# Kernel optimization log

Measured on AMD Instinct MI355X. Metric: run time of the kernel, lower is better.

Reference implementation:

```python
import jax, jax.numpy as jnp
import numpy as np

D_ATOM, D_MODEL, H = 128, 512, 4
D_H = D_ATOM // H
D_FF = 4 * D_ATOM
EPS = 1e-5


def _ln(x, g, b):
    m = jnp.mean(x, axis=-1, keepdims=True)
    v = jnp.mean((x - m) ** 2, axis=-1, keepdims=True)
    return (x - m) / jnp.sqrt(v + EPS) * g + b


def setup_inputs() -> dict:
    key = jax.random.key(0)
    ks = jax.random.split(key, 20)
    B, N_ATOM, N_PAIRS, N_TOK = 2, 2048, 16384, 512
    c_atom = jax.random.normal(ks[0], (B, N_ATOM, D_ATOM), dtype=jnp.float32)
    p_lm = jax.random.normal(ks[1], (B, N_PAIRS, 16), dtype=jnp.float32)
    p_lm_idx = jax.random.randint(ks[2], (B, N_PAIRS, 2), 0, N_ATOM, dtype=jnp.int32)
    token_idx = jnp.sort(jax.random.randint(ks[3], (B, N_ATOM), 0, N_TOK, dtype=jnp.int32), axis=-1)
    s = 0.05
    w = lambda k, sh: jax.random.normal(k, sh, dtype=jnp.float32) * s
    return {
        'c_atom': c_atom, 'p_lm': p_lm, 'p_lm_idx': p_lm_idx,
        'token_idx': token_idx, 'n_tokens': N_TOK,
        'ln_attn_g': jnp.ones((D_ATOM,), jnp.float32), 'ln_attn_b': jnp.zeros((D_ATOM,), jnp.float32),
        'w_q': w(ks[4], (D_ATOM, D_ATOM)), 'w_k': w(ks[5], (D_ATOM, D_ATOM)),
        'w_v': w(ks[6], (D_ATOM, D_ATOM)), 'w_g': w(ks[7], (D_ATOM, D_ATOM)),
        'w_o': w(ks[8], (D_ATOM, D_ATOM)),
        'pb_w': w(ks[9], (16, H)), 'pb_b': jnp.zeros((H,), jnp.float32),
        'ln_ff_g': jnp.ones((D_ATOM,), jnp.float32), 'ln_ff_b': jnp.zeros((D_ATOM,), jnp.float32),
        'sw_w1': w(ks[10], (D_ATOM, D_FF)), 'sw_w2': w(ks[11], (D_ATOM, D_FF)),
        'sw_w3': w(ks[12], (D_FF, D_ATOM)),
        'tok_w': w(ks[13], (D_ATOM, D_MODEL)), 'tok_b': jnp.zeros((D_MODEL,), jnp.float32),
    }


def reference(c_atom, p_lm, p_lm_idx, token_idx, n_tokens,
              ln_attn_g, ln_attn_b, w_q, w_k, w_v, w_g, w_o, pb_w, pb_b,
              ln_ff_g, ln_ff_b, sw_w1, sw_w2, sw_w3, tok_w, tok_b):
    B, N, _ = c_atom.shape
    q_n = _ln(c_atom, ln_attn_g, ln_attn_b)
    Q = (q_n @ w_q).reshape(B, N, H, D_H)
    K = (q_n @ w_k).reshape(B, N, H, D_H)
    V = (q_n @ w_v).reshape(B, N, H, D_H)
    G = q_n @ w_g  # (B, N, d_atom)

    scores = jnp.einsum('bihd,bjhd->bhij', Q, K) / jnp.sqrt(jnp.float32(D_H))

    bias = p_lm @ pb_w + pb_b  # (B, P, H)
    def scat(src, dst, b_):
        return jnp.zeros((H, N, N), b_.dtype).at[:, src, dst].set(b_.T)
    pair_bias = jax.vmap(scat)(p_lm_idx[..., 0], p_lm_idx[..., 1], bias)
    scores = scores + pair_bias

    token_mask = token_idx[:, :, None] == token_idx[:, None, :]  # (B,N,N)
    scores = jnp.where(token_mask[:, None], scores, -jnp.inf)
    attn = jax.nn.softmax(scores, axis=-1)
    attn = jnp.nan_to_num(attn)

    att_out = jnp.einsum('bhij,bjhd->bihd', attn, V).reshape(B, N, D_ATOM)
    q = c_atom + jax.nn.sigmoid(G) * (att_out @ w_o)
    h = _ln(q, ln_ff_g, ln_ff_b)
    q = q + (jax.nn.silu(h @ sw_w1) * (h @ sw_w2)) @ sw_w3
    atom_feat = q @ tok_w + tok_b  # (B, N, d_model)

    seg = (token_idx + jnp.arange(B, dtype=token_idx.dtype)[:, None] * n_tokens).reshape(-1)
    sums = jax.ops.segment_sum(atom_feat.reshape(B * N, D_MODEL), seg, num_segments=B * n_tokens)
    cnts = jax.ops.segment_sum(jnp.ones((B * N,), atom_feat.dtype), seg, num_segments=B * n_tokens)
    out = sums / jnp.maximum(cnts, 1.0)[:, None]
    return out.reshape(B, n_tokens, D_MODEL)
```

## Files before the change

### kernel.cpp

```cpp
#include <hip/hip_runtime.h>
#include <hip/hip_bf16.h>
#include <math.h>

#define B_     2
#define N_     2048
#define DA     128
#define H_     4
#define DH     32
#define DFF    512
#define DM     512
#define NT     512
#define NP     16384
#define MAXL   32
#define LDSP   136

typedef short bf16x8 __attribute__((ext_vector_type(8)));
typedef float f32x4  __attribute__((ext_vector_type(4)));

__device__ __forceinline__ short bf16r(float x) {
    union { float f; unsigned u; } v; v.f = x;
    unsigned r = v.u + 0x7FFFu + ((v.u >> 16) & 1u);
    return (short)(r >> 16);
}
__device__ __forceinline__ float bf2f(short h) {
    union { unsigned u; float f; } v;
    v.u = ((unsigned)(unsigned short)h) << 16;
    return v.f;
}

__global__ __launch_bounds__(1024) void setup_kernel(
        const float* __restrict__ wq, const float* __restrict__ wk,
        const float* __restrict__ wv, const float* __restrict__ wg,
        const float* __restrict__ wo, const float* __restrict__ w1,
        const float* __restrict__ w2, const float* __restrict__ w3,
        const float* __restrict__ tw, const int* __restrict__ tok,
        const int* __restrict__ pidx,
        short* __restrict__ pqkvg, short* __restrict__ pwo,
        short* __restrict__ pw12, short* __restrict__ pw3,
        short* __restrict__ ptok,
        int* __restrict__ cnt, int* __restrict__ tst,
        int* __restrict__ win) {
    __shared__ int c[1024];
    __shared__ int sb[1024];
    if (blockIdx.x < 42) {
        int gid = blockIdx.x * 1024 + threadIdx.x;
        int lane = gid & 63;
        int grp = gid >> 6;
        int quad = lane >> 4, nn = lane & 15;
        const float* src; short* dst; int stride;
        if (grp < 128) {
            int g = grp; int kt = g & 3, nt = g >> 2;
            int n = nt * 16 + nn;
            const float* w = (n < 128) ? wq : (n < 256) ? wk : (n < 384) ? wv : wg;
            src = w + (kt * 32 + quad * 8) * 128 + (n & 127);
            dst = pqkvg + (g * 64 + lane) * 8;
            stride = 128;
        } else if (grp < 160) {
            int g = grp - 128; int kt = g & 3, nt = g >> 2;
            src = wo + (kt * 32 + quad * 8) * 128 + nt * 16 + nn;
            dst = pwo + (g * 64 + lane) * 8;
            stride = 128;
        } else if (grp < 416) {
            int g = grp - 160; int kt = g & 3, nt = g >> 2;
            int n = nt * 16 + nn;
            src = ((n & 1) ? w2 : w1) + (kt * 32 + quad * 8) * 512 + (n >> 1);
            dst = pw12 + (g * 64 + lane) * 8;
            stride = 512;
        } else if (grp < 544) {
            int g = grp - 416; int kt = g & 15, nt = g >> 4;
            src = w3 + (kt * 32 + quad * 8) * 128 + nt * 16 + nn;
            dst = pw3 + (g * 64 + lane) * 8;
            stride = 128;
        } else {
            int g = grp - 544; int kt = g & 3, nt = g >> 2;
            src = tw + (kt * 32 + quad * 8) * 512 + nt * 16 + nn;
            dst = ptok + (g * 64 + lane) * 8;
            stride = 512;
        }
#pragma unroll
        for (int j = 0; j < 8; j++) dst[j] = bf16r(src[j * stride]);
    } else if (blockIdx.x == 42) {
        int tid = threadIdx.x;
        c[tid] = 0;
        __syncthreads();
#pragma unroll
        for (int i = 0; i < 4; i++) {
            int idx = tid + i * 1024;
            int b = idx >> 11;
            atomicAdd(&c[b * NT + tok[idx]], 1);
        }
        __syncthreads();
        int t = tid & (NT - 1);
        int v = c[tid];
        int* cur = c;
        int* alt = sb;
        for (int d = 1; d < NT; d <<= 1) {
            int y = cur[tid];
            if (t >= d) y += cur[tid - d];
            alt[tid] = y;
            __syncthreads();
            int* tmp = cur; cur = alt; alt = tmp;
        }
        tst[tid] = cur[tid] - v;
        cnt[tid] = v;
    } else {
        int p = (blockIdx.x - 43) * 1024 + threadIdx.x;
        int b = p >> 14, pp = p & (NP - 1);
        int src = pidx[p * 2], dst = pidx[p * 2 + 1];
        if (tok[b * N_ + src] == tok[b * N_ + dst])
            atomicMax(&win[(b * N_ + src) * MAXL + (dst & 31)], pp + 1);
    }
}

__device__ __forceinline__ void ln_to_lds(const float* __restrict__ x,
                                          const float* __restrict__ g,
                                          const float* __restrict__ b,
                                          short* __restrict__ lds) {
    int t = threadIdx.x;
    int row = t >> 2, sub = t & 3;
    const float* xr = x + row * DA + sub * 32;
    float4 v[8];
    float s = 0.f, sq = 0.f;
#pragma unroll
    for (int i = 0; i < 8; i++) {
        v[i] = *(const float4*)(xr + i * 4);
        s  += v[i].x + v[i].y + v[i].z + v[i].w;
        sq += v[i].x * v[i].x + v[i].y * v[i].y + v[i].z * v[i].z + v[i].w * v[i].w;
    }
    s += __shfl_xor(s, 1); sq += __shfl_xor(sq, 1);
    s += __shfl_xor(s, 2); sq += __shfl_xor(sq, 2);
    float mean = s * (1.f / 128.f);
    float var = sq * (1.f / 128.f) - mean * mean;
    float inv = rsqrtf(var + 1e-5f);
    const float* gp = g + sub * 32;
    const float* bp = b + sub * 32;
    short* dst = lds + row * LDSP + sub * 32;
#pragma unroll
    for (int i = 0; i < 8; i++) {
        dst[i * 4 + 0] = bf16r((v[i].x - mean) * inv * gp[i * 4 + 0] + bp[i * 4 + 0]);
        dst[i * 4 + 1] = bf16r((v[i].y - mean) * inv * gp[i * 4 + 1] + bp[i * 4 + 1]);
        dst[i * 4 + 2] = bf16r((v[i].z - mean) * inv * gp[i * 4 + 2] + bp[i * 4 + 2]);
        dst[i * 4 + 3] = bf16r((v[i].w - mean) * inv * gp[i * 4 + 3] + bp[i * 4 + 3]);
    }
}

template<int K, int NTT>
__device__ __forceinline__ void gemm_lds(const short* __restrict__ Alds,
                                         const short* __restrict__ Bp,
                                         int nt0, int lane, f32x4* acc) {
    constexpr int KT = K / 32;
    const short* arow = Alds + (lane & 15) * LDSP + (lane >> 4) * 8;
    const short* bbase = Bp + nt0 * KT * 512 + lane * 8;
#pragma unroll
    for (int kt = 0; kt < KT; kt++) {
        bf16x8 a = *(const bf16x8*)(arow + kt * 32);
#pragma unroll
        for (int nt = 0; nt < NTT; nt++) {
            bf16x8 b = *(const bf16x8*)(bbase + (nt * KT + kt) * 512);
            acc[nt] = __builtin_amdgcn_mfma_f32_16x16x32_bf16(a, b, acc[nt], 0, 0, 0);
        }
    }
}

template<int K, int NTT>
__device__ __forceinline__ void gemm_glb(const short* __restrict__ A,
                                         const short* __restrict__ Bp,
                                         int m0, int nt0, int lane, f32x4* acc) {
    constexpr int KT = K / 32;
    const short* arow = A + (m0 + (lane & 15)) * K + (lane >> 4) * 8;
    const short* bbase = Bp + nt0 * KT * 512 + lane * 8;
#pragma unroll
    for (int kt = 0; kt < KT; kt++) {
        bf16x8 a = *(const bf16x8*)(arow + kt * 32);
#pragma unroll
        for (int nt = 0; nt < NTT; nt++) {
            bf16x8 b = *(const bf16x8*)(bbase + (nt * KT + kt) * 512);
            acc[nt] = __builtin_amdgcn_mfma_f32_16x16x32_bf16(a, b, acc[nt], 0, 0, 0);
        }
    }
}

__global__ __launch_bounds__(256) void lnqkvg_mfma(const float* __restrict__ c_atom,
                                                   const float* __restrict__ lg,
                                                   const float* __restrict__ lb,
                                                   const short* __restrict__ Bp,
                                                   float* __restrict__ out) {
    __shared__ short alds[64 * LDSP];
    int base = blockIdx.x * 64;
    ln_to_lds(c_atom + base * DA, lg, lb, alds);
    __syncthreads();
    int lane = threadIdx.x & 63;
    int wave = threadIdx.x >> 6;
    int nt0 = blockIdx.y * 8;
    f32x4 acc[8];
#pragma unroll
    for (int i = 0; i < 8; i++)
#pragma unroll
        for (int r = 0; r < 4; r++) acc[i][r] = 0.f;
    gemm_lds<128, 8>(alds + wave * 16 * LDSP, Bp, nt0, lane, acc);
    int r0 = base + wave * 16 + ((lane >> 4) << 2);
    int cc = lane & 15;
#pragma unroll
    for (int nt = 0; nt < 8; nt++) {
        int col = (nt0 + nt) * 16 + cc;
#pragma unroll
        for (int r = 0; r < 4; r++) out[(r0 + r) * 512 + col] = acc[nt][r];
    }
}

__global__ __launch_bounds__(128) void attn_kernel(const float* __restrict__ qkvg,
                                                   const int* __restrict__ tok,
                                                   const int* __restrict__ tst,
                                                   const int* __restrict__ cnt,
                                                   const int* __restrict__ winner,
                                                   const float* __restrict__ plm,
                                                   const float* __restrict__ pbw,
                                                   const float* __restrict__ pbb,
                                                   short* __restrict__ atth) {
    __shared__ float sc[H_][MAXL];
    int blk = blockIdx.x;
    int b = blk >> 11;
    int h = threadIdx.x >> 5, d = threadIdx.x & 31;
    int t = tok[blk];
    int start = tst[b * NT + t];
    int L = cnt[b * NT + t];
    if (L > MAXL) L = MAXL;
    float qv = qkvg[blk * 512 + h * DH + d];
    const float scale = 0.17677669529663687f;
    for (int jj = 0; jj < L; jj++) {
        int j = b * N_ + start + jj;
        float kv = qkvg[j * 512 + 128 + h * DH + d];
        float s = qv * kv;
#pragma unroll
        for (int m = 16; m; m >>= 1) s += __shfl_xor(s, m, 32);
        s *= scale;
        int pp1 = winner[blk * MAXL + ((start + jj) & 31)];
        if (pp1 > 0) {
            const float* pl = plm + (b * NP + pp1 - 1) * 16;
            float bsum = pbb[h];
#pragma unroll
            for (int f = 0; f < 16; f++) bsum += pl[f] * pbw[f * H_ + h];
            s += bsum;
        }
        if (d == 0) sc[h][jj] = s;
    }
    __syncthreads();
    float mx = -1e30f;
    for (int jj = 0; jj < L; jj++) mx = fmaxf(mx, sc[h][jj]);
    float denom = 0.f, acc = 0.f;
    for (int jj = 0; jj < L; jj++) {
        float pj = expf(sc[h][jj] - mx);
        denom += pj;
        acc += pj * qkvg[(b * N_ + start + jj) * 512 + 256 + h * DH + d];
    }
    atth[blk * DA + h * DH + d] = bf16r(acc / denom);
}

__global__ __launch_bounds__(256) void oplnffn1_mfma(const short* __restrict__ atth,
                                                     const short* __restrict__ pwo,
                                                     const float* __restrict__ qkvg,
                                                     const float* __restrict__ c_atom,
                                                     const float* __restrict__ lg,
                                                     const float* __restrict__ lb,
                                                     const short* __restrict__ pw12,
                                                     float* __restrict__ qbuf,
                                                     short* __restrict__ u) {
    __shared__ short alds[64 * LDSP];
    int lane = threadIdx.x & 63;
    int wave = threadIdx.x >> 6;
    int base = blockIdx.x * 64;
    int m0 = base + wave * 16;
    int quad = lane >> 4, cc = lane & 15;

    f32x4 acc[8];
#pragma unroll
    for (int i = 0; i < 8; i++)
#pragma unroll
        for (int r = 0; r < 4; r++) acc[i][r] = 0.f;
    gemm_glb<128, 8>(atth, pwo, m0, 0, lane, acc);

    float rsum[4], rsq[4];
#pragma unroll
    for (int r = 0; r < 4; r++) {
        int row = m0 + quad * 4 + r;
        float s = 0.f, sq = 0.f;
#pragma unroll
        for (int nt = 0; nt < 8; nt++) {
            int col = nt * 16 + cc;
            float g = qkvg[row * 512 + 384 + col];
            float sg = 1.f / (1.f + expf(-g));
            float val = c_atom[row * DA + col] + sg * acc[nt][r];
            acc[nt][r] = val;
            s += val; sq += val * val;
            if (blockIdx.y == 0) qbuf[row * DA + col] = val;
        }
        rsum[r] = s; rsq[r] = sq;
    }
#pragma unroll
    for (int m = 1; m < 16; m <<= 1) {
#pragma unroll
        for (int r = 0; r < 4; r++) {
            rsum[r] += __shfl_xor(rsum[r], m);
            rsq[r]  += __shfl_xor(rsq[r], m);
        }
    }
#pragma unroll
    for (int r = 0; r < 4; r++) {
        float mean = rsum[r] * (1.f / 128.f);
        float var = rsq[r] * (1.f / 128.f) - mean * mean;
        float inv = rsqrtf(var + 1e-5f);
        int lrow = wave * 16 + quad * 4 + r;
#pragma unroll
        for (int nt = 0; nt < 8; nt++) {
            int col = nt * 16 + cc;
            alds[lrow * LDSP + col] = bf16r((acc[nt][r] - mean) * inv * lg[col] + lb[col]);
        }
    }
    __syncthreads();

    int nt0 = blockIdx.y * 16;
    f32x4 acc2[16];
#pragma unroll
    for (int i = 0; i < 16; i++)
#pragma unroll
        for (int r = 0; r < 4; r++) acc2[i][r] = 0.f;
    gemm_lds<128, 16>(alds + wave * 16 * LDSP, pw12, nt0, lane, acc2);
    int r0 = m0 + quad * 4;
#pragma unroll
    for (int nt = 0; nt < 16; nt++) {
        int col8 = (nt0 + nt) * 8 + (cc >> 1);
#pragma unroll
        for (int r = 0; r < 4; r++) {
            float v = acc2[nt][r];
            float p = __shfl_xor(v, 1);
            if (!(lane & 1)) {
                float sil = v / (1.f + expf(-v));
                u[(r0 + r) * DFF + col8] = bf16r(sil * p);
            }
        }
    }
}

__global__ __launch_bounds__(128) void ffn2_mfma(const short* __restrict__ u,
                                                 const short* __restrict__ Bp,
                                                 const float* __restrict__ qbuf,
                                                 short* __restrict__ q2h) {
    int lane = threadIdx.x & 63;
    int m0 = blockIdx.x * 32 + (threadIdx.x >> 6) * 16;
    int nt0 = blockIdx.y * 4;
    f32x4 acc[4];
#pragma unroll
    for (int i = 0; i < 4; i++)
#pragma unroll
        for (int r = 0; r < 4; r++) acc[i][r] = 0.f;
    gemm_glb<512, 4>(u, Bp, m0, nt0, lane, acc);
    int r0 = m0 + ((lane >> 4) << 2);
    int cc = lane & 15;
#pragma unroll
    for (int nt = 0; nt < 4; nt++) {
        int col = (nt0 + nt) * 16 + cc;
#pragma unroll
        for (int r = 0; r < 4; r++) {
            int row = r0 + r;
            q2h[row * DA + col] = bf16r(qbuf[row * DA + col] + acc[nt][r]);
        }
    }
}

__global__ __launch_bounds__(256) void tokmean_mfma(const short* __restrict__ q2h,
                                                    const int* __restrict__ tst,
                                                    const int* __restrict__ cnt,
                                                    const short* __restrict__ Bp,
                                                    const float* __restrict__ tb,
                                                    float* __restrict__ out) {
    __shared__ short alds[64 * LDSP];
    int tid = threadIdx.x;
    int tt = tid >> 2, sub = tid & 3;
    int token = blockIdx.x * 64 + tt;
    int start = tst[token], n = cnt[token];
    int b = token >> 9;
    float accm[32];
#pragma unroll
    for (int i = 0; i < 32; i++) accm[i] = 0.f;
    for (int a = 0; a < n; a++) {
        const short* rp = q2h + (b * N_ + start + a) * DA + sub * 32;
#pragma unroll
        for (int v8 = 0; v8 < 4; v8++) {
            bf16x8 v = *(const bf16x8*)(rp + v8 * 8);
#pragma unroll
            for (int j = 0; j < 8; j++) accm[v8 * 8 + j] += bf2f(v[j]);
        }
    }
    float inv = (n > 0) ? 1.f / (float)n : 0.f;
    short* dst = alds + tt * LDSP + sub * 32;
#pragma unroll
    for (int i = 0; i < 32; i++) dst[i] = bf16r(accm[i] * inv);
    __syncthreads();

    int lane = tid & 63;
    int wave = tid >> 6;
    int nt0 = blockIdx.y * 4;
    f32x4 acc[4];
#pragma unroll
    for (int i = 0; i < 4; i++)
#pragma unroll
        for (int r = 0; r < 4; r++) acc[i][r] = 0.f;
    gemm_lds<128, 4>(alds + wave * 16 * LDSP, Bp, nt0, lane, acc);
    int r0 = blockIdx.x * 64 + wave * 16 + ((lane >> 4) << 2);
    int cc = lane & 15;
#pragma unroll
    for (int nt = 0; nt < 4; nt++) {
        int col = (nt0 + nt) * 16 + cc;
        float bv = tb[col];
#pragma unroll
        for (int r = 0; r < 4; r++) out[(size_t)(r0 + r) * DM + col] = acc[nt][r] + bv;
    }
}

extern "C" void kernel_launch(void* const* d_in, const int* in_sizes, int n_in,
                              void* d_out, int out_size, void* d_ws, size_t ws_size,
                              hipStream_t stream) {
    const float* c_atom  = (const float*)d_in[0];
    const float* p_lm    = (const float*)d_in[1];
    const int*   p_idx   = (const int*)d_in[2];
    const int*   tok     = (const int*)d_in[3];
    const float* ln_a_g  = (const float*)d_in[5];
    const float* ln_a_b  = (const float*)d_in[6];
    const float* w_q     = (const float*)d_in[7];
    const float* w_k     = (const float*)d_in[8];
    const float* w_v     = (const float*)d_in[9];
    const float* w_g     = (const float*)d_in[10];
    const float* w_o     = (const float*)d_in[11];
    const float* pb_w    = (const float*)d_in[12];
    const float* pb_b    = (const float*)d_in[13];
    const float* ln_f_g  = (const float*)d_in[14];
    const float* ln_f_b  = (const float*)d_in[15];
    const float* sw_w1   = (const float*)d_in[16];
    const float* sw_w2   = (const float*)d_in[17];
    const float* sw_w3   = (const float*)d_in[18];
    const float* tok_w   = (const float*)d_in[19];
    const float* tok_b   = (const float*)d_in[20];
    float* out = (float*)d_out;

    float* ws = (float*)d_ws;
    int*   cnt   = (int*)ws;
    int*   tst   = cnt + 1024;
    int*   win   = tst + 1024;
    short* pqkvg = (short*)(win + 131072);
    short* pwo   = pqkvg + 65536;
    short* pw12  = pwo + 16384;
    short* pw3   = pw12 + 131072;
    short* ptok  = pw3 + 65536;
    short* atth  = ptok + 65536;
    float* qbuf  = (float*)(atth + 524288);
    float* qkvg  = qbuf + 524288;
    short* uh    = (short*)(qkvg + 2097152);
    short* q2h   = atth;

    setup_kernel<<<75, 1024, 0, stream>>>(w_q, w_k, w_v, w_g, w_o, sw_w1, sw_w2,
                                          sw_w3, tok_w, tok, p_idx,
                                          pqkvg, pwo, pw12, pw3, ptok,
                                          cnt, tst, win);

    lnqkvg_mfma<<<dim3(64, 4), 256, 0, stream>>>(c_atom, ln_a_g, ln_a_b, pqkvg, qkvg);

    attn_kernel<<<B_ * N_, 128, 0, stream>>>(qkvg, tok, tst, cnt, win,
                                             p_lm, pb_w, pb_b, atth);

    oplnffn1_mfma<<<dim3(64, 4), 256, 0, stream>>>(atth, pwo, qkvg, c_atom,
                                                   ln_f_g, ln_f_b, pw12, qbuf, uh);

    ffn2_mfma<<<dim3(128, 2), 128, 0, stream>>>(uh, pw3, qbuf, q2h);

    tokmean_mfma<<<dim3(16, 8), 256, 0, stream>>>(q2h, tst, cnt, ptok, tok_b, out);
}
```

Before: 162.0 us.

## Fuse all stages into one cooperative persistent kernel with grid syncs

Replaces the six separate kernel launches (setup, LN+QKVG GEMM, attention, out-proj+LN+FFN1, FFN2, token mean) with a single cooperative kernel of 256 blocks that runs each stage in turn, separated by grid.sync(). The goal is to remove per-launch overhead and inter-kernel gaps on a small workload. In exchange, each stage is limited to a fixed 256x256 grid: attention and setup work are looped over in grid-stride fashion, and FFN2 is re-tiled so each wave computes fewer output tiles. Grid-wide barriers carry their own cost.

```diff
diff --git a/kernel.cpp b/kernel.cpp
--- a/kernel.cpp
+++ b/kernel.cpp
@@ -1,6 +1,9 @@
 #include <hip/hip_runtime.h>
 #include <hip/hip_bf16.h>
+#include <hip/hip_cooperative_groups.h>
 #include <math.h>
+
+namespace cg = cooperative_groups;
 
 #define B_     2
 #define N_     2048
@@ -28,87 +31,39 @@
     return v.f;
 }
 
-__global__ __launch_bounds__(1024) void setup_kernel(
-        const float* __restrict__ wq, const float* __restrict__ wk,
-        const float* __restrict__ wv, const float* __restrict__ wg,
-        const float* __restrict__ wo, const float* __restrict__ w1,
-        const float* __restrict__ w2, const float* __restrict__ w3,
-        const float* __restrict__ tw, const int* __restrict__ tok,
-        const int* __restrict__ pidx,
-        short* __restrict__ pqkvg, short* __restrict__ pwo,
-        short* __restrict__ pw12, short* __restrict__ pw3,
-        short* __restrict__ ptok,
-        int* __restrict__ cnt, int* __restrict__ tst,
-        int* __restrict__ win) {
-    __shared__ int c[1024];
-    __shared__ int sb[1024];
-    if (blockIdx.x < 42) {
-        int gid = blockIdx.x * 1024 + threadIdx.x;
-        int lane = gid & 63;
-        int grp = gid >> 6;
-        int quad = lane >> 4, nn = lane & 15;
-        const float* src; short* dst; int stride;
-        if (grp < 128) {
-            int g = grp; int kt = g & 3, nt = g >> 2;
-            int n = nt * 16 + nn;
-            const float* w = (n < 128) ? wq : (n < 256) ? wk : (n < 384) ? wv : wg;
-            src = w + (kt * 32 + quad * 8) * 128 + (n & 127);
-            dst = pqkvg + (g * 64 + lane) * 8;
-            stride = 128;
-        } else if (grp < 160) {
-            int g = grp - 128; int kt = g & 3, nt = g >> 2;
-            src = wo + (kt * 32 + quad * 8) * 128 + nt * 16 + nn;
-            dst = pwo + (g * 64 + lane) * 8;
-            stride = 128;
-        } else if (grp < 416) {
-            int g = grp - 160; int kt = g & 3, nt = g >> 2;
-            int n = nt * 16 + nn;
-            src = ((n & 1) ? w2 : w1) + (kt * 32 + quad * 8) * 512 + (n >> 1);
-            dst = pw12 + (g * 64 + lane) * 8;
-            stride = 512;
-        } else if (grp < 544) {
-            int g = grp - 416; int kt = g & 15, nt = g >> 4;
-            src = w3 + (kt * 32 + quad * 8) * 128 + nt * 16 + nn;
-            dst = pw3 + (g * 64 + lane) * 8;
-            stride = 128;
-        } else {
-            int g = grp - 544; int kt = g & 3, nt = g >> 2;
-            src = tw + (kt * 32 + quad * 8) * 512 + nt * 16 + nn;
-            dst = ptok + (g * 64 + lane) * 8;
-            stride = 512;
-        }
-#pragma unroll
-        for (int j = 0; j < 8; j++) dst[j] = bf16r(src[j * stride]);
-    } else if (blockIdx.x == 42) {
-        int tid = threadIdx.x;
-        c[tid] = 0;
-        __syncthreads();
-#pragma unroll
-        for (int i = 0; i < 4; i++) {
-            int idx = tid + i * 1024;
-            int b = idx >> 11;
-            atomicAdd(&c[b * NT + tok[idx]], 1);
-        }
-        __syncthreads();
-        int t = tid & (NT - 1);
-        int v = c[tid];
-        int* cur = c;
-        int* alt = sb;
-        for (int d = 1; d < NT; d <<= 1) {
-            int y = cur[tid];
-            if (t >= d) y += cur[tid - d];
-            alt[tid] = y;
-            __syncthreads();
-            int* tmp = cur; cur = alt; alt = tmp;
-        }
-        tst[tid] = cur[tid] - v;
-        cnt[tid] = v;
-    } else {
-        int p = (blockIdx.x - 43) * 1024 + threadIdx.x;
-        int b = p >> 14, pp = p & (NP - 1);
-        int src = pidx[p * 2], dst = pidx[p * 2 + 1];
-        if (tok[b * N_ + src] == tok[b * N_ + dst])
-            atomicMax(&win[(b * N_ + src) * MAXL + (dst & 31)], pp + 1);
+template<int K, int NTT>
+__device__ __forceinline__ void gemm_lds(const short* __restrict__ Alds,
+                                         const short* __restrict__ Bp,
+                                         int nt0, int lane, f32x4* acc) {
+    constexpr int KT = K / 32;
+    const short* arow = Alds + (lane & 15) * LDSP + (lane >> 4) * 8;
+    const short* bbase = Bp + nt0 * KT * 512 + lane * 8;
+#pragma unroll
+    for (int kt = 0; kt < KT; kt++) {
+        bf16x8 a = *(const bf16x8*)(arow + kt * 32);
+#pragma unroll
+        for (int nt = 0; nt < NTT; nt++) {
+            bf16x8 b = *(const bf16x8*)(bbase + (nt * KT + kt) * 512);
+            acc[nt] = __builtin_amdgcn_mfma_f32_16x16x32_bf16(a, b, acc[nt], 0, 0, 0);
+        }
+    }
+}
+
+template<int K, int NTT>
+__device__ __forceinline__ void gemm_glb(const short* __restrict__ A,
+                                         const short* __restrict__ Bp,
+                                         int m0, int nt0, int lane, f32x4* acc) {
+    constexpr int KT = K / 32;
+    const short* arow = A + (m0 + (lane & 15)) * K + (lane >> 4) * 8;
+    const short* bbase = Bp + nt0 * KT * 512 + lane * 8;
+#pragma unroll
+    for (int kt = 0; kt < KT; kt++) {
+        bf16x8 a = *(const bf16x8*)(arow + kt * 32);
+#pragma unroll
+        for (int nt = 0; nt < NTT; nt++) {
+            bf16x8 b = *(const bf16x8*)(bbase + (nt * KT + kt) * 512);
+            acc[nt] = __builtin_amdgcn_mfma_f32_16x16x32_bf16(a, b, acc[nt], 0, 0, 0);
+        }
     }
 }
 
@@ -144,304 +99,325 @@
     }
 }
 
-template<int K, int NTT>
-__device__ __forceinline__ void gemm_lds(const short* __restrict__ Alds,
-                                         const short* __restrict__ Bp,
-                                         int nt0, int lane, f32x4* acc) {
-    constexpr int KT = K / 32;
-    const short* arow = Alds + (lane & 15) * LDSP + (lane >> 4) * 8;
-    const short* bbase = Bp + nt0 * KT * 512 + lane * 8;
-#pragma unroll
-    for (int kt = 0; kt < KT; kt++) {
-        bf16x8 a = *(const bf16x8*)(arow + kt * 32);
-#pragma unroll
-        for (int nt = 0; nt < NTT; nt++) {
-            bf16x8 b = *(const bf16x8*)(bbase + (nt * KT + kt) * 512);
-            acc[nt] = __builtin_amdgcn_mfma_f32_16x16x32_bf16(a, b, acc[nt], 0, 0, 0);
-        }
-    }
-}
-
-template<int K, int NTT>
-__device__ __forceinline__ void gemm_glb(const short* __restrict__ A,
-                                         const short* __restrict__ Bp,
-                                         int m0, int nt0, int lane, f32x4* acc) {
-    constexpr int KT = K / 32;
-    const short* arow = A + (m0 + (lane & 15)) * K + (lane >> 4) * 8;
-    const short* bbase = Bp + nt0 * KT * 512 + lane * 8;
-#pragma unroll
-    for (int kt = 0; kt < KT; kt++) {
-        bf16x8 a = *(const bf16x8*)(arow + kt * 32);
-#pragma unroll
-        for (int nt = 0; nt < NTT; nt++) {
-            bf16x8 b = *(const bf16x8*)(bbase + (nt * KT + kt) * 512);
-            acc[nt] = __builtin_amdgcn_mfma_f32_16x16x32_bf16(a, b, acc[nt], 0, 0, 0);
-        }
-    }
-}
-
-__global__ __launch_bounds__(256) void lnqkvg_mfma(const float* __restrict__ c_atom,
-                                                   const float* __restrict__ lg,
-                                                   const float* __restrict__ lb,
-                                                   const short* __restrict__ Bp,
-                                                   float* __restrict__ out) {
-    __shared__ short alds[64 * LDSP];
-    int base = blockIdx.x * 64;
-    ln_to_lds(c_atom + base * DA, lg, lb, alds);
-    __syncthreads();
-    int lane = threadIdx.x & 63;
-    int wave = threadIdx.x >> 6;
-    int nt0 = blockIdx.y * 8;
-    f32x4 acc[8];
-#pragma unroll
-    for (int i = 0; i < 8; i++)
-#pragma unroll
-        for (int r = 0; r < 4; r++) acc[i][r] = 0.f;
-    gemm_lds<128, 8>(alds + wave * 16 * LDSP, Bp, nt0, lane, acc);
-    int r0 = base + wave * 16 + ((lane >> 4) << 2);
-    int cc = lane & 15;
-#pragma unroll
-    for (int nt = 0; nt < 8; nt++) {
-        int col = (nt0 + nt) * 16 + cc;
-#pragma unroll
-        for (int r = 0; r < 4; r++) out[(r0 + r) * 512 + col] = acc[nt][r];
-    }
-}
-
-__global__ __launch_bounds__(128) void attn_kernel(const float* __restrict__ qkvg,
-                                                   const int* __restrict__ tok,
-                                                   const int* __restrict__ tst,
-                                                   const int* __restrict__ cnt,
-                                                   const int* __restrict__ winner,
-                                                   const float* __restrict__ plm,
-                                                   const float* __restrict__ pbw,
-                                                   const float* __restrict__ pbb,
-                                                   short* __restrict__ atth) {
-    __shared__ float sc[H_][MAXL];
+struct MegaArgs {
+    const float *c_atom, *plm; const int *pidx, *tok;
+    const float *lag, *lab;
+    const float *wq, *wk, *wv, *wg, *wo, *pbw, *pbb, *lfg, *lfb, *w1, *w2, *w3, *tw, *tb;
+    int *cnt, *tst, *win;
+    short *pqkvg, *pwo, *pw12, *pw3, *ptok, *atth;
+    float *qbuf, *qkvg; short *uh, *q2h; float *outp;
+};
+
+__global__ __launch_bounds__(256) void mega_kernel(MegaArgs a) {
+    cg::grid_group grid = cg::this_grid();
+    __shared__ __align__(16) char smem[64 * LDSP * 2];
+    short* alds = (short*)smem;
     int blk = blockIdx.x;
-    int b = blk >> 11;
-    int h = threadIdx.x >> 5, d = threadIdx.x & 31;
-    int t = tok[blk];
-    int start = tst[b * NT + t];
-    int L = cnt[b * NT + t];
-    if (L > MAXL) L = MAXL;
-    float qv = qkvg[blk * 512 + h * DH + d];
-    const float scale = 0.17677669529663687f;
-    for (int jj = 0; jj < L; jj++) {
-        int j = b * N_ + start + jj;
-        float kv = qkvg[j * 512 + 128 + h * DH + d];
-        float s = qv * kv;
-#pragma unroll
-        for (int m = 16; m; m >>= 1) s += __shfl_xor(s, m, 32);
-        s *= scale;
-        int pp1 = winner[blk * MAXL + ((start + jj) & 31)];
-        if (pp1 > 0) {
-            const float* pl = plm + (b * NP + pp1 - 1) * 16;
-            float bsum = pbb[h];
-#pragma unroll
-            for (int f = 0; f < 16; f++) bsum += pl[f] * pbw[f * H_ + h];
-            s += bsum;
-        }
-        if (d == 0) sc[h][jj] = s;
-    }
-    __syncthreads();
-    float mx = -1e30f;
-    for (int jj = 0; jj < L; jj++) mx = fmaxf(mx, sc[h][jj]);
-    float denom = 0.f, acc = 0.f;
-    for (int jj = 0; jj < L; jj++) {
-        float pj = expf(sc[h][jj] - mx);
-        denom += pj;
-        acc += pj * qkvg[(b * N_ + start + jj) * 512 + 256 + h * DH + d];
-    }
-    atth[blk * DA + h * DH + d] = bf16r(acc / denom);
-}
-
-__global__ __launch_bounds__(256) void oplnffn1_mfma(const short* __restrict__ atth,
-                                                     const short* __restrict__ pwo,
-                                                     const float* __restrict__ qkvg,
-                                                     const float* __restrict__ c_atom,
-                                                     const float* __restrict__ lg,
-                                                     const float* __restrict__ lb,
-                                                     const short* __restrict__ pw12,
-                                                     float* __restrict__ qbuf,
-                                                     short* __restrict__ u) {
-    __shared__ short alds[64 * LDSP];
-    int lane = threadIdx.x & 63;
-    int wave = threadIdx.x >> 6;
-    int base = blockIdx.x * 64;
-    int m0 = base + wave * 16;
-    int quad = lane >> 4, cc = lane & 15;
-
-    f32x4 acc[8];
-#pragma unroll
-    for (int i = 0; i < 8; i++)
-#pragma unroll
-        for (int r = 0; r < 4; r++) acc[i][r] = 0.f;
-    gemm_glb<128, 8>(atth, pwo, m0, 0, lane, acc);
-
-    float rsum[4], rsq[4];
-#pragma unroll
-    for (int r = 0; r < 4; r++) {
-        int row = m0 + quad * 4 + r;
-        float s = 0.f, sq = 0.f;
-#pragma unroll
-        for (int nt = 0; nt < 8; nt++) {
-            int col = nt * 16 + cc;
-            float g = qkvg[row * 512 + 384 + col];
-            float sg = 1.f / (1.f + expf(-g));
-            float val = c_atom[row * DA + col] + sg * acc[nt][r];
-            acc[nt][r] = val;
-            s += val; sq += val * val;
-            if (blockIdx.y == 0) qbuf[row * DA + col] = val;
-        }
-        rsum[r] = s; rsq[r] = sq;
-    }
-#pragma unroll
-    for (int m = 1; m < 16; m <<= 1) {
-#pragma unroll
-        for (int r = 0; r < 4; r++) {
-            rsum[r] += __shfl_xor(rsum[r], m);
-            rsq[r]  += __shfl_xor(rsq[r], m);
-        }
-    }
-#pragma unroll
-    for (int r = 0; r < 4; r++) {
-        float mean = rsum[r] * (1.f / 128.f);
-        float var = rsq[r] * (1.f / 128.f) - mean * mean;
-        float inv = rsqrtf(var + 1e-5f);
-        int lrow = wave * 16 + quad * 4 + r;
-#pragma unroll
-        for (int nt = 0; nt < 8; nt++) {
-            int col = nt * 16 + cc;
-            alds[lrow * LDSP + col] = bf16r((acc[nt][r] - mean) * inv * lg[col] + lb[col]);
-        }
-    }
-    __syncthreads();
-
-    int nt0 = blockIdx.y * 16;
-    f32x4 acc2[16];
-#pragma unroll
-    for (int i = 0; i < 16; i++)
-#pragma unroll
-        for (int r = 0; r < 4; r++) acc2[i][r] = 0.f;
-    gemm_lds<128, 16>(alds + wave * 16 * LDSP, pw12, nt0, lane, acc2);
-    int r0 = m0 + quad * 4;
-#pragma unroll
-    for (int nt = 0; nt < 16; nt++) {
-        int col8 = (nt0 + nt) * 8 + (cc >> 1);
-#pragma unroll
-        for (int r = 0; r < 4; r++) {
-            float v = acc2[nt][r];
-            float p = __shfl_xor(v, 1);
-            if (!(lane & 1)) {
-                float sil = v / (1.f + expf(-v));
-                u[(r0 + r) * DFF + col8] = bf16r(sil * p);
-            }
-        }
-    }
-}
-
-__global__ __launch_bounds__(128) void ffn2_mfma(const short* __restrict__ u,
-                                                 const short* __restrict__ Bp,
-                                                 const float* __restrict__ qbuf,
-                                                 short* __restrict__ q2h) {
-    int lane = threadIdx.x & 63;
-    int m0 = blockIdx.x * 32 + (threadIdx.x >> 6) * 16;
-    int nt0 = blockIdx.y * 4;
-    f32x4 acc[4];
-#pragma unroll
-    for (int i = 0; i < 4; i++)
-#pragma unroll
-        for (int r = 0; r < 4; r++) acc[i][r] = 0.f;
-    gemm_glb<512, 4>(u, Bp, m0, nt0, lane, acc);
-    int r0 = m0 + ((lane >> 4) << 2);
-    int cc = lane & 15;
-#pragma unroll
-    for (int nt = 0; nt < 4; nt++) {
-        int col = (nt0 + nt) * 16 + cc;
-#pragma unroll
-        for (int r = 0; r < 4; r++) {
-            int row = r0 + r;
-            q2h[row * DA + col] = bf16r(qbuf[row * DA + col] + acc[nt][r]);
-        }
-    }
-}
-
-__global__ __launch_bounds__(256) void tokmean_mfma(const short* __restrict__ q2h,
-                                                    const int* __restrict__ tst,
-                                                    const int* __restrict__ cnt,
-                                                    const short* __restrict__ Bp,
-                                                    const float* __restrict__ tb,
-                                                    float* __restrict__ out) {
-    __shared__ short alds[64 * LDSP];
     int tid = threadIdx.x;
-    int tt = tid >> 2, sub = tid & 3;
-    int token = blockIdx.x * 64 + tt;
-    int start = tst[token], n = cnt[token];
-    int b = token >> 9;
-    float accm[32];
-#pragma unroll
-    for (int i = 0; i < 32; i++) accm[i] = 0.f;
-    for (int a = 0; a < n; a++) {
-        const short* rp = q2h + (b * N_ + start + a) * DA + sub * 32;
-#pragma unroll
-        for (int v8 = 0; v8 < 4; v8++) {
-            bf16x8 v = *(const bf16x8*)(rp + v8 * 8);
-#pragma unroll
-            for (int j = 0; j < 8; j++) accm[v8 * 8 + j] += bf2f(v[j]);
-        }
-    }
-    float inv = (n > 0) ? 1.f / (float)n : 0.f;
-    short* dst = alds + tt * LDSP + sub * 32;
-#pragma unroll
-    for (int i = 0; i < 32; i++) dst[i] = bf16r(accm[i] * inv);
-    __syncthreads();
-
+    int gtid = blk * 256 + tid;
     int lane = tid & 63;
     int wave = tid >> 6;
-    int nt0 = blockIdx.y * 4;
-    f32x4 acc[4];
-#pragma unroll
-    for (int i = 0; i < 4; i++)
-#pragma unroll
-        for (int r = 0; r < 4; r++) acc[i][r] = 0.f;
-    gemm_lds<128, 4>(alds + wave * 16 * LDSP, Bp, nt0, lane, acc);
-    int r0 = blockIdx.x * 64 + wave * 16 + ((lane >> 4) << 2);
-    int cc = lane & 15;
-#pragma unroll
-    for (int nt = 0; nt < 4; nt++) {
-        int col = (nt0 + nt) * 16 + cc;
-        float bv = tb[col];
-#pragma unroll
-        for (int r = 0; r < 4; r++) out[(size_t)(r0 + r) * DM + col] = acc[nt][r] + bv;
+    int quad = lane >> 4, cc = lane & 15;
+
+    for (int item = gtid; item < 43008 + 32768; item += 65536) {
+        if (item < 43008) {
+            int plane = item & 63;
+            int grp = item >> 6;
+            int pq = plane >> 4, nn = plane & 15;
+            const float* src; short* dst; int stride;
+            if (grp < 128) {
+                int g = grp; int kt = g & 3, nt = g >> 2;
+                int n = nt * 16 + nn;
+                const float* w = (n < 128) ? a.wq : (n < 256) ? a.wk : (n < 384) ? a.wv : a.wg;
+                src = w + (kt * 32 + pq * 8) * 128 + (n & 127);
+                dst = a.pqkvg + (g * 64 + plane) * 8;
+                stride = 128;
+            } else if (grp < 160) {
+                int g = grp - 128; int kt = g & 3, nt = g >> 2;
+                src = a.wo + (kt * 32 + pq * 8) * 128 + nt * 16 + nn;
+                dst = a.pwo + (g * 64 + plane) * 8;
+                stride = 128;
+            } else if (grp < 416) {
+                int g = grp - 160; int kt = g & 3, nt = g >> 2;
+                int n = nt * 16 + nn;
+                src = ((n & 1) ? a.w2 : a.w1) + (kt * 32 + pq * 8) * 512 + (n >> 1);
+                dst = a.pw12 + (g * 64 + plane) * 8;
+                stride = 512;
+            } else if (grp < 544) {
+                int g = grp - 416; int kt = g & 15, nt = g >> 4;
+                src = a.w3 + (kt * 32 + pq * 8) * 128 + nt * 16 + nn;
+                dst = a.pw3 + (g * 64 + plane) * 8;
+                stride = 128;
+            } else {
+                int g = grp - 544; int kt = g & 3, nt = g >> 2;
+                src = a.tw + (kt * 32 + pq * 8) * 512 + nt * 16 + nn;
+                dst = a.ptok + (g * 64 + plane) * 8;
+                stride = 512;
+            }
+#pragma unroll
+            for (int j = 0; j < 8; j++) dst[j] = bf16r(src[j * stride]);
+        } else {
+            int p = item - 43008;
+            int b = p >> 14, pp = p & (NP - 1);
+            int src = a.pidx[p * 2], dst = a.pidx[p * 2 + 1];
+            if (a.tok[b * N_ + src] == a.tok[b * N_ + dst])
+                atomicMax(&a.win[(b * N_ + src) * MAXL + (dst & 31)], pp + 1);
+        }
+    }
+    if (blk == 255) {
+        int* c = (int*)smem;
+        int* sb = c + 1024;
+#pragma unroll
+        for (int j = 0; j < 4; j++) c[tid + j * 256] = 0;
+        __syncthreads();
+#pragma unroll
+        for (int i = 0; i < 16; i++) {
+            int idx = tid + i * 256;
+            atomicAdd(&c[(idx >> 11) * NT + a.tok[idx]], 1);
+        }
+        __syncthreads();
+        int vorig[4];
+#pragma unroll
+        for (int j = 0; j < 4; j++) vorig[j] = c[tid + j * 256];
+        int* cur = c;
+        int* alt = sb;
+        for (int d = 1; d < NT; d <<= 1) {
+            int y[4];
+#pragma unroll
+            for (int j = 0; j < 4; j++) {
+                int i = tid + j * 256;
+                int t = i & (NT - 1);
+                y[j] = cur[i];
+                if (t >= d) y[j] += cur[i - d];
+            }
+            __syncthreads();
+#pragma unroll
+            for (int j = 0; j < 4; j++) alt[tid + j * 256] = y[j];
+            __syncthreads();
+            int* tmp = cur; cur = alt; alt = tmp;
+        }
+#pragma unroll
+        for (int j = 0; j < 4; j++) {
+            int i = tid + j * 256;
+            a.tst[i] = cur[i] - vorig[j];
+            a.cnt[i] = vorig[j];
+        }
+    }
+    grid.sync();
+
+    {
+        int bx = blk & 63, by = blk >> 6;
+        int base = bx * 64;
+        ln_to_lds(a.c_atom + base * DA, a.lag, a.lab, alds);
+        __syncthreads();
+        int nt0 = by * 8;
+        f32x4 acc[8];
+#pragma unroll
+        for (int i = 0; i < 8; i++)
+#pragma unroll
+            for (int r = 0; r < 4; r++) acc[i][r] = 0.f;
+        gemm_lds<128, 8>(alds + wave * 16 * LDSP, a.pqkvg, nt0, lane, acc);
+        int r0 = base + wave * 16 + quad * 4;
+#pragma unroll
+        for (int nt = 0; nt < 8; nt++) {
+            int col = (nt0 + nt) * 16 + cc;
+#pragma unroll
+            for (int r = 0; r < 4; r++) a.qkvg[(r0 + r) * 512 + col] = acc[nt][r];
+        }
+    }
+    grid.sync();
+
+    {
+        float* sc = (float*)smem;
+        int half = tid >> 7;
+        int ltid = tid & 127;
+        int h = ltid >> 5, d = ltid & 31;
+        float* schh = sc + (half * H_ + h) * MAXL;
+        const float scale = 0.17677669529663687f;
+        for (int it = 0; it < 8; it++) {
+            int ai = blk * 16 + it * 2 + half;
+            int b = ai >> 11;
+            int t = a.tok[ai];
+            int start = a.tst[b * NT + t];
+            int L = a.cnt[b * NT + t];
+            if (L > MAXL) L = MAXL;
+            float qv = a.qkvg[ai * 512 + h * DH + d];
+            for (int jj = 0; jj < L; jj++) {
+                int j = b * N_ + start + jj;
+                float kv = a.qkvg[j * 512 + 128 + h * DH + d];
+                float s = qv * kv;
+#pragma unroll
+                for (int m = 16; m; m >>= 1) s += __shfl_xor(s, m, 32);
+                s *= scale;
+                int pp1 = a.win[ai * MAXL + ((start + jj) & 31)];
+                if (pp1 > 0) {
+                    const float* pl = a.plm + (b * NP + pp1 - 1) * 16;
+                    float bsum = a.pbb[h];
+#pragma unroll
+                    for (int f = 0; f < 16; f++) bsum += pl[f] * a.pbw[f * H_ + h];
+                    s += bsum;
+                }
+                if (d == 0) schh[jj] = s;
+            }
+            __syncthreads();
+            float mx = -1e30f;
+            for (int jj = 0; jj < L; jj++) mx = fmaxf(mx, schh[jj]);
+            float denom = 0.f, acc = 0.f;
+            for (int jj = 0; jj < L; jj++) {
+                float pj = expf(schh[jj] - mx);
+                denom += pj;
+                acc += pj * a.qkvg[(b * N_ + start + jj) * 512 + 256 + h * DH + d];
+            }
+            a.atth[ai * DA + h * DH + d] = bf16r(acc / denom);
+            __syncthreads();
+        }
+    }
+    grid.sync();
+
+    {
+        int bx = blk & 63, by = blk >> 6;
+        int base = bx * 64;
+        int m0 = base + wave * 16;
+        f32x4 acc[8];
+#pragma unroll
+        for (int i = 0; i < 8; i++)
+#pragma unroll
+            for (int r = 0; r < 4; r++) acc[i][r] = 0.f;
+        gemm_glb<128, 8>(a.atth, a.pwo, m0, 0, lane, acc);
+
+        float rsum[4], rsq[4];
+#pragma unroll
+        for (int r = 0; r < 4; r++) {
+            int row = m0 + quad * 4 + r;
+            float s = 0.f, sq = 0.f;
+#pragma unroll
+            for (int nt = 0; nt < 8; nt++) {
+                int col = nt * 16 + cc;
+                float g = a.qkvg[row * 512 + 384 + col];
+                float sg = 1.f / (1.f + expf(-g));
+                float val = a.c_atom[row * DA + col] + sg * acc[nt][r];
+                acc[nt][r] = val;
+                s += val; sq += val * val;
+                if (by == 0) a.qbuf[row * DA + col] = val;
+            }
+            rsum[r] = s; rsq[r] = sq;
+        }
+#pragma unroll
+        for (int m = 1; m < 16; m <<= 1) {
+#pragma unroll
+            for (int r = 0; r < 4; r++) {
+                rsum[r] += __shfl_xor(rsum[r], m);
+                rsq[r]  += __shfl_xor(rsq[r], m);
+            }
+        }
+#pragma unroll
+        for (int r = 0; r < 4; r++) {
+            float mean = rsum[r] * (1.f / 128.f);
+            float var = rsq[r] * (1.f / 128.f) - mean * mean;
+            float inv = rsqrtf(var + 1e-5f);
+            int lrow = wave * 16 + quad * 4 + r;
+#pragma unroll
+            for (int nt = 0; nt < 8; nt++) {
+                int col = nt * 16 + cc;
+                alds[lrow * LDSP + col] =
+                    bf16r((acc[nt][r] - mean) * inv * a.lfg[col] + a.lfb[col]);
+            }
+        }
+        __syncthreads();
+
+        int nt0 = by * 16;
+        f32x4 acc2[16];
+#pragma unroll
+        for (int i = 0; i < 16; i++)
+#pragma unroll
+            for (int r = 0; r < 4; r++) acc2[i][r] = 0.f;
+        gemm_lds<128, 16>(alds + wave * 16 * LDSP, a.pw12, nt0, lane, acc2);
+        int r0 = m0 + quad * 4;
+#pragma unroll
+        for (int nt = 0; nt < 16; nt++) {
+            int col8 = (nt0 + nt) * 8 + (cc >> 1);
+#pragma unroll
+            for (int r = 0; r < 4; r++) {
+                float v = acc2[nt][r];
+                float p = __shfl_xor(v, 1);
+                if (!(lane & 1)) {
+                    float sil = v / (1.f + expf(-v));
+                    a.uh[(r0 + r) * DFF + col8] = bf16r(sil * p);
+                }
+            }
+        }
+    }
+    grid.sync();
+
+    {
+        int w = blk * 4 + wave;
+        int m0 = (w >> 2) * 16;
+        int nt0 = (w & 3) * 2;
+        f32x4 acc[2];
+#pragma unroll
+        for (int i = 0; i < 2; i++)
+#pragma unroll
+            for (int r = 0; r < 4; r++) acc[i][r] = 0.f;
+        gemm_glb<512, 2>(a.uh, a.pw3, m0, nt0, lane, acc);
+        int r0 = m0 + quad * 4;
+#pragma unroll
+        for (int nt = 0; nt < 2; nt++) {
+            int col = (nt0 + nt) * 16 + cc;
+#pragma unroll
+            for (int r = 0; r < 4; r++) {
+                int row = r0 + r;
+                a.q2h[row * DA + col] = bf16r(a.qbuf[row * DA + col] + acc[nt][r]);
+            }
+        }
+    }
+    grid.sync();
+
+    if (blk < 128) {
+        int bx = blk & 15, by = blk >> 4;
+        int tt = tid >> 2, sub = tid & 3;
+        int token = bx * 64 + tt;
+        int start = a.tst[token], n = a.cnt[token];
+        int b = token >> 9;
+        float accm[32];
+#pragma unroll
+        for (int i = 0; i < 32; i++) accm[i] = 0.f;
+        for (int at = 0; at < n; at++) {
+            const short* rp = a.q2h + (b * N_ + start + at) * DA + sub * 32;
+#pragma unroll
+            for (int v8 = 0; v8 < 4; v8++) {
+                bf16x8 v = *(const bf16x8*)(rp + v8 * 8);
+#pragma unroll
+                for (int j = 0; j < 8; j++) accm[v8 * 8 + j] += bf2f(v[j]);
+            }
+        }
+        float inv = (n > 0) ? 1.f / (float)n : 0.f;
+        short* dst = alds + tt * LDSP + sub * 32;
+#pragma unroll
+        for (int i = 0; i < 32; i++) dst[i] = bf16r(accm[i] * inv);
+        __syncthreads();
+
+        int nt0 = by * 4;
+        f32x4 acc[4];
+#pragma unroll
+        for (int i = 0; i < 4; i++)
+#pragma unroll
+            for (int r = 0; r < 4; r++) acc[i][r] = 0.f;
+        gemm_lds<128, 4>(alds + wave * 16 * LDSP, a.ptok, nt0, lane, acc);
+        int r0 = bx * 64 + wave * 16 + quad * 4;
+#pragma unroll
+        for (int nt = 0; nt < 4; nt++) {
+            int col = (nt0 + nt) * 16 + cc;
+            float bv = a.tb[col];
+#pragma unroll
+            for (int r = 0; r < 4; r++)
+                a.outp[(size_t)(r0 + r) * DM + col] = acc[nt][r] + bv;
+        }
     }
 }
 
 extern "C" void kernel_launch(void* const* d_in, const int* in_sizes, int n_in,
                               void* d_out, int out_size, void* d_ws, size_t ws_size,
                               hipStream_t stream) {
-    const float* c_atom  = (const float*)d_in[0];
-    const float* p_lm    = (const float*)d_in[1];
-    const int*   p_idx   = (const int*)d_in[2];
-    const int*   tok     = (const int*)d_in[3];
-    const float* ln_a_g  = (const float*)d_in[5];
-    const float* ln_a_b  = (const float*)d_in[6];
-    const float* w_q     = (const float*)d_in[7];
-    const float* w_k     = (const float*)d_in[8];
-    const float* w_v     = (const float*)d_in[9];
-    const float* w_g     = (const float*)d_in[10];
-    const float* w_o     = (const float*)d_in[11];
-    const float* pb_w    = (const float*)d_in[12];
-    const float* pb_b    = (const float*)d_in[13];
-    const float* ln_f_g  = (const float*)d_in[14];
-    const float* ln_f_b  = (const float*)d_in[15];
-    const float* sw_w1   = (const float*)d_in[16];
-    const float* sw_w2   = (const float*)d_in[17];
-    const float* sw_w3   = (const float*)d_in[18];
-    const float* tok_w   = (const float*)d_in[19];
-    const float* tok_b   = (const float*)d_in[20];
-    float* out = (float*)d_out;
-
     float* ws = (float*)d_ws;
     int*   cnt   = (int*)ws;
     int*   tst   = cnt + 1024;
@@ -457,20 +433,33 @@
     short* uh    = (short*)(qkvg + 2097152);
     short* q2h   = atth;
 
-    setup_kernel<<<75, 1024, 0, stream>>>(w_q, w_k, w_v, w_g, w_o, sw_w1, sw_w2,
-                                          sw_w3, tok_w, tok, p_idx,
-                                          pqkvg, pwo, pw12, pw3, ptok,
-                                          cnt, tst, win);
-
-    lnqkvg_mfma<<<dim3(64, 4), 256, 0, stream>>>(c_atom, ln_a_g, ln_a_b, pqkvg, qkvg);
-
-    attn_kernel<<<B_ * N_, 128, 0, stream>>>(qkvg, tok, tst, cnt, win,
-                                             p_lm, pb_w, pb_b, atth);
-
-    oplnffn1_mfma<<<dim3(64, 4), 256, 0, stream>>>(atth, pwo, qkvg, c_atom,
-                                                   ln_f_g, ln_f_b, pw12, qbuf, uh);
-
-    ffn2_mfma<<<dim3(128, 2), 128, 0, stream>>>(uh, pw3, qbuf, q2h);
-
-    tokmean_mfma<<<dim3(16, 8), 256, 0, stream>>>(q2h, tst, cnt, ptok, tok_b, out);
-}
+    MegaArgs a;
+    a.c_atom = (const float*)d_in[0];
+    a.plm    = (const float*)d_in[1];
+    a.pidx   = (const int*)d_in[2];
+    a.tok    = (const int*)d_in[3];
+    a.lag    = (const float*)d_in[5];
+    a.lab    = (const float*)d_in[6];
+    a.wq     = (const float*)d_in[7];
+    a.wk     = (const float*)d_in[8];
+    a.wv     = (const float*)d_in[9];
+    a.wg     = (const float*)d_in[10];
+    a.wo     = (const float*)d_in[11];
+    a.pbw    = (const float*)d_in[12];
+    a.pbb    = (const float*)d_in[13];
+    a.lfg    = (const float*)d_in[14];
+    a.lfb    = (const float*)d_in[15];
+    a.w1     = (const float*)d_in[16];
+    a.w2     = (const float*)d_in[17];
+    a.w3     = (const float*)d_in[18];
+    a.tw     = (const float*)d_in[19];
+    a.tb     = (const float*)d_in[20];
+    a.cnt = cnt; a.tst = tst; a.win = win;
+    a.pqkvg = pqkvg; a.pwo = pwo; a.pw12 = pw12; a.pw3 = pw3; a.ptok = ptok;
+    a.atth = atth; a.qbuf = qbuf; a.qkvg = qkvg; a.uh = uh; a.q2h = q2h;
+    a.outp = (float*)d_out;
+
+    void* kargs[] = { &a };
+    hipLaunchCooperativeKernel((void*)mega_kernel, dim3(256), dim3(256),
+                               kargs, 0, stream);
+}
```

Result: slower. 356.3 us (+119.9%).
